# Kernel optimization log

Measured on AMD Instinct MI355X. Metric: run time of the kernel, lower is better.

## Reference

```python
import jax, jax.numpy as jnp
import numpy as np

N, E, D = 100_000, 1_250_000, 64
EPS = 1e-8

def setup_inputs() -> dict:
    key = jax.random.key(0)
    ks = jax.random.split(key, 8)
    h = jax.random.normal(ks[0], (N, D), jnp.float32)
    eig = jax.random.normal(ks[1], (E, 1), jnp.float32)          # per-edge vector field
    snorm_n = jax.random.uniform(ks[2], (N, 1), jnp.float32)     # node norm
    src = jax.random.randint(ks[3], (E,), 0, N)
    dst = jax.random.randint(ks[4], (E,), 0, N)
    # pretrans: Linear(2D -> D); posttrans: Linear((3+1)*D -> D); torch Linear weight is [out, in]
    W1 = jax.random.normal(ks[5], (D, 2 * D), jnp.float32) / np.sqrt(2.0 * D)
    b1 = jnp.zeros((D,), jnp.float32)
    W2 = jax.random.normal(ks[6], (D, 4 * D), jnp.float32) / np.sqrt(4.0 * D)
    b2 = jnp.zeros((D,), jnp.float32)
    gamma = jnp.ones((D,), jnp.float32)   # BatchNorm1d weight
    beta = jnp.zeros((D,), jnp.float32)   # BatchNorm1d bias
    return dict(h=h, eig=eig, snorm_n=snorm_n, src=src, dst=dst,
                W1=W1, b1=b1, W2=W2, b2=b2, gamma=gamma, beta=beta)

def reference(h, eig, snorm_n, src, dst, W1, b1, W2, b2, gamma, beta):
    seg = lambda x: jax.ops.segment_sum(x, dst, num_segments=N)
    # pretrans on edges: MLP(cat[h_src, h_dst])
    z2 = jnp.concatenate([h[src], h[dst]], axis=1)   # [E, 2D]
    e = z2 @ W1.T + b1                                # [E, D]
    deg = seg(jnp.ones((E, 1), e.dtype))              # [N, 1]
    # aggregator: mean
    agg_mean = seg(e) / jnp.maximum(deg, 1.0)
    # aggregator: max (empty segments -> 0)
    agg_max = jax.ops.segment_max(e, dst, num_segments=N)
    agg_max = jnp.where(deg > 0, agg_max, 0.0)
    # aggregator: directional derivative dir_dx
    absum = seg(jnp.abs(eig))                         # [N, 1] sum of |vf| per node
    w = eig / (absum[dst] + EPS)                      # [E, 1] normalized weights
    agg_dir = jnp.abs(seg(e * w) - seg(w) * h)        # [N, D]
    # posttrans on nodes
    hc = jnp.concatenate([h, agg_mean, agg_max, agg_dir], axis=1)  # [N, 4D]
    h2 = (hc @ W2.T + b2) * snorm_n
    # BatchNorm1d (training mode: batch stats, biased variance)
    mu = jnp.mean(h2, axis=0)
    var = jnp.var(h2, axis=0)
    h2 = (h2 - mu) * jax.lax.rsqrt(var + 1e-5) * gamma + beta
    h2 = jax.nn.relu(h2)
    # residual (in_dim == out_dim); dropout p=0 is identity
    return h + h2
```

## Files before the change

kernel.cpp:

```cpp
#include <hip/hip_runtime.h>
#include <math.h>

__device__ __forceinline__ float bf2f(unsigned short s) {
    return __uint_as_float(((unsigned)s) << 16);
}
__device__ __forceinline__ unsigned short f2bf(float f) {
    unsigned u = __float_as_uint(f);
    unsigned r = (u + 0x7fffu + ((u >> 16) & 1u)) >> 16;
    return (unsigned short)r;
}

typedef __attribute__((ext_vector_type(8))) short short8v;
typedef __attribute__((ext_vector_type(4))) float f32x4;


__device__ __forceinline__ void edge_rank_body(
    int bid, const int* __restrict__ dst, int* __restrict__ cursor,
    int* __restrict__ rank, int E)
{
    int t = bid * 256 + threadIdx.x;
    int base = t * 8;
    if (base >= E) return;
    if (base + 8 <= E) {
        int4 d0 = *(const int4*)(dst + base);
        int4 d1 = *(const int4*)(dst + base + 4);
        int r0 = atomicAdd(&cursor[d0.x], 1);
        int r1 = atomicAdd(&cursor[d0.y], 1);
        int r2 = atomicAdd(&cursor[d0.z], 1);
        int r3 = atomicAdd(&cursor[d0.w], 1);
        int r4 = atomicAdd(&cursor[d1.x], 1);
        int r5 = atomicAdd(&cursor[d1.y], 1);
        int r6 = atomicAdd(&cursor[d1.z], 1);
        int r7 = atomicAdd(&cursor[d1.w], 1);
        *(int4*)(rank + base)     = make_int4(r0, r1, r2, r3);
        *(int4*)(rank + base + 4) = make_int4(r4, r5, r6, r7);
    } else {
        for (int e = base; e < E; ++e)
            rank[e] = atomicAdd(&cursor[dst[e]], 1);
    }
}

__device__ __forceinline__ void hb_cast_body(
    int bid, const float* __restrict__ h, unsigned short* __restrict__ hb, long total8)
{
    long idx = (long)bid * 256 + threadIdx.x;
    if (idx >= total8) return;
    const float4 a = *(const float4*)(h + idx * 8);
    const float4 b = *(const float4*)(h + idx * 8 + 4);
    union { unsigned short s[8]; uint4 v4; } pk;
    pk.s[0] = f2bf(a.x); pk.s[1] = f2bf(a.y); pk.s[2] = f2bf(a.z); pk.s[3] = f2bf(a.w);
    pk.s[4] = f2bf(b.x); pk.s[5] = f2bf(b.y); pk.s[6] = f2bf(b.z); pk.s[7] = f2bf(b.w);
    *(uint4*)(hb + idx * 8) = pk.v4;
}

__device__ __forceinline__ void wprep_body(
    int bid, const float* __restrict__ W1, const float* __restrict__ W2,
    unsigned short* __restrict__ w1bf, unsigned short* __restrict__ w2bf)
{
    int idx = bid * 256 + threadIdx.x;
    if (idx < 128 * 64) {
        int c = idx >> 6, j = idx & 63;
        float val = (c < 64) ? W1[c * 128 + j] : W1[(c - 64) * 128 + 64 + j];
        w1bf[idx] = f2bf(val);
    } else if (idx < 128 * 64 + 64 * 256) {
        int k = idx - 128 * 64;
        w2bf[k] = f2bf(W2[k]);
    }
}

__device__ __forceinline__ void csr_scatter_body(
    int bid, const int* __restrict__ src, const int* __restrict__ dst,
    const float* __restrict__ eig, const int* __restrict__ rank,
    const int* __restrict__ offs, int2* __restrict__ csr, int E)
{
    int e = bid * 256 + threadIdx.x;
    if (e < E) {
        int dn = dst[e];
        int p = offs[dn] + rank[e];
        csr[p] = make_int2(src[e], __float_as_int(eig[e]));
    }
}

__device__ __forceinline__ void uv_mfma_body(
    int bid, const unsigned short* __restrict__ hb, const unsigned short* __restrict__ w1bf,
    const float* __restrict__ b1,
    unsigned short* __restrict__ u, unsigned short* __restrict__ v)
{
    int lane = threadIdx.x & 63;
    int wv = threadIdx.x >> 6;
    int lr = lane & 15;
    int lg = lane >> 4;

    short8v a[2][2];
#pragma unroll
    for (int rt = 0; rt < 2; ++rt)
#pragma unroll
        for (int s = 0; s < 2; ++s)
            a[rt][s] = *(const short8v*)(w1bf + (size_t)(wv * 32 + rt * 16 + lr) * 64 + s * 32 + lg * 8);

    float b1v[2][4];
#pragma unroll
    for (int rt = 0; rt < 2; ++rt) {
        if (wv >= 2) {
            float4 t4 = *(const float4*)(b1 + (wv - 2) * 32 + rt * 16 + lg * 4);
            b1v[rt][0] = t4.x; b1v[rt][1] = t4.y; b1v[rt][2] = t4.z; b1v[rt][3] = t4.w;
        } else {
            b1v[rt][0] = b1v[rt][1] = b1v[rt][2] = b1v[rt][3] = 0.f;
        }
    }

    unsigned short* outp = (wv < 2) ? u : v;
    int coff0 = (wv & 1) * 32 + lg * 4;

    int n0 = bid * 64;

    short8v bb[2][2];
    {
        const unsigned short* hp = hb + (size_t)(n0 + lr) * 64 + lg * 8;
        bb[0][0] = *(const short8v*)(hp);
        bb[0][1] = *(const short8v*)(hp + 32);
    }
#pragma unroll
    for (int t = 0; t < 4; ++t) {
        int cur = t & 1, nxt = cur ^ 1;
        if (t < 3) {
            const unsigned short* hp = hb + (size_t)(n0 + (t + 1) * 16 + lr) * 64 + lg * 8;
            bb[nxt][0] = *(const short8v*)(hp);
            bb[nxt][1] = *(const short8v*)(hp + 32);
        }
        f32x4 acc0 = {0.f, 0.f, 0.f, 0.f}, acc1 = {0.f, 0.f, 0.f, 0.f};
        acc0 = __builtin_amdgcn_mfma_f32_16x16x32_bf16(a[0][0], bb[cur][0], acc0, 0, 0, 0);
        acc1 = __builtin_amdgcn_mfma_f32_16x16x32_bf16(a[1][0], bb[cur][0], acc1, 0, 0, 0);
        acc0 = __builtin_amdgcn_mfma_f32_16x16x32_bf16(a[0][1], bb[cur][1], acc0, 0, 0, 0);
        acc1 = __builtin_amdgcn_mfma_f32_16x16x32_bf16(a[1][1], bb[cur][1], acc1, 0, 0, 0);
        int node = n0 + t * 16 + lr;
        union { unsigned short s[4]; uint2 v2; } pk;
#pragma unroll
        for (int r = 0; r < 4; ++r) pk.s[r] = f2bf(acc0[r] + b1v[0][r]);
        *(uint2*)(outp + (size_t)node * 64 + coff0) = pk.v2;
#pragma unroll
        for (int r = 0; r < 4; ++r) pk.s[r] = f2bf(acc1[r] + b1v[1][r]);
        *(uint2*)(outp + (size_t)node * 64 + coff0 + 16) = pk.v2;
    }
}

__global__ __launch_bounds__(256) void mega1_kernel(
    const int* __restrict__ dst, int* __restrict__ cursor, int* __restrict__ rank, int E,
    const float* __restrict__ h, unsigned short* __restrict__ hb, long total8,
    const float* __restrict__ W1, const float* __restrict__ W2,
    unsigned short* __restrict__ w1bf, unsigned short* __restrict__ w2bf,
    int nrank, int ncast)
{
    int b = blockIdx.x;
    if (b < nrank)              edge_rank_body(b, dst, cursor, rank, E);
    else if (b < nrank + ncast) hb_cast_body(b - nrank, h, hb, total8);
    else                        wprep_body(b - nrank - ncast, W1, W2, w1bf, w2bf);
}

__global__ __launch_bounds__(256) void mega2_kernel(
    const unsigned short* __restrict__ hb, const unsigned short* __restrict__ w1bf,
    const float* __restrict__ b1, unsigned short* __restrict__ u, unsigned short* __restrict__ v,
    const int* __restrict__ src, const int* __restrict__ dst, const float* __restrict__ eig,
    const int* __restrict__ rank, const int* __restrict__ offs, int2* __restrict__ csr,
    int E, int nuv)
{
    int b = blockIdx.x;
    if (b < nuv) uv_mfma_body(b, hb, w1bf, b1, u, v);
    else         csr_scatter_body(b - nuv, src, dst, eig, rank, offs, csr, E);
}

__global__ __launch_bounds__(256) void block_reduce_kernel(
    const int* __restrict__ deg, int* __restrict__ bsum, int N)
{
    __shared__ int sd[256];
    int t = threadIdx.x;
    int i = blockIdx.x * 256 + t;
    sd[t] = (i < N) ? deg[i] : 0;
    __syncthreads();
    for (int s = 128; s > 0; s >>= 1) {
        if (t < s) sd[t] += sd[t + s];
        __syncthreads();
    }
    if (t == 0) bsum[blockIdx.x] = sd[0];
}

__global__ __launch_bounds__(1024) void scan_bsums_kernel(
    const int* __restrict__ bsum, int* __restrict__ bscan, int nb)
{
    __shared__ int sd[1024];
    int t = threadIdx.x;
    int own = (t < nb) ? bsum[t] : 0;
    sd[t] = own;
    __syncthreads();
    for (int off = 1; off < 1024; off <<= 1) {
        int v = (t >= off) ? sd[t - off] : 0;
        __syncthreads();
        sd[t] += v;
        __syncthreads();
    }
    if (t < nb) bscan[t] = sd[t] - own;
}

__global__ __launch_bounds__(256) void block_scan_kernel(
    const int* __restrict__ deg, const int* __restrict__ bscan,
    int* __restrict__ offs, int N)
{
    __shared__ int sd[256];
    int t = threadIdx.x;
    int i = blockIdx.x * 256 + t;
    int myv = (i < N) ? deg[i] : 0;
    sd[t] = myv;
    __syncthreads();
    for (int off = 1; off < 256; off <<= 1) {
        int v = (t >= off) ? sd[t - off] : 0;
        __syncthreads();
        sd[t] += v;
        __syncthreads();
    }
    if (i < N) {
        offs[i] = sd[t] - myv + bscan[blockIdx.x];
    }
}

__global__ __launch_bounds__(256) void agg_kernel(
    const unsigned short* __restrict__ u, const unsigned short* __restrict__ v,
    const unsigned short* __restrict__ hb,
    const int* __restrict__ offs, const int* __restrict__ degi,
    const int2* __restrict__ csr,
    unsigned short* __restrict__ agg, int N)
{
    int gw = (blockIdx.x * 256 + threadIdx.x) >> 6;
    int lane = threadIdx.x & 63;
    int n = __builtin_amdgcn_readfirstlane(gw);
    if (n >= N) return;
    int dn  = __builtin_amdgcn_readfirstlane(degi[n]);
    int beg = __builtin_amdgcn_readfirstlane(offs[n]);

    float vl = bf2f(v[(size_t)n * 64 + lane]);
    float hl = bf2f(hb[(size_t)n * 64 + lane]);

    const int2* ep = csr + beg;
    float accs = 0.f, accd = 0.f, accm = -3.402823466e38f;
    float pa = 0.f, ps = 0.f;

    int j = 0;
    for (; j + 4 <= dn; j += 4) {
        int2 r0 = ep[j], r1 = ep[j + 1], r2 = ep[j + 2], r3 = ep[j + 3];
        float u0 = bf2f(u[(size_t)r0.x * 64 + lane]);
        float u1 = bf2f(u[(size_t)r1.x * 64 + lane]);
        float u2 = bf2f(u[(size_t)r2.x * 64 + lane]);
        float u3 = bf2f(u[(size_t)r3.x * 64 + lane]);
        float w0 = __int_as_float(r0.y), w1 = __int_as_float(r1.y);
        float w2_ = __int_as_float(r2.y), w3 = __int_as_float(r3.y);
        pa += (fabsf(w0) + fabsf(w1)) + (fabsf(w2_) + fabsf(w3));
        ps += (w0 + w1) + (w2_ + w3);
        accs += (u0 + u1) + (u2 + u3);
        accm = fmaxf(accm, fmaxf(fmaxf(u0, u1), fmaxf(u2, u3)));
        accd = fmaf(w0, u0, fmaf(w1, u1, fmaf(w2_, u2, fmaf(w3, u3, accd))));
    }
    for (; j < dn; ++j) {
        int2 r0 = ep[j];
        float u0 = bf2f(u[(size_t)r0.x * 64 + lane]);
        float w0 = __int_as_float(r0.y);
        pa += fabsf(w0);
        ps += w0;
        accs += u0;
        accm = fmaxf(accm, u0);
        accd = fmaf(w0, u0, accd);
    }

    float inv_ab = 1.f / (pa + 1e-8f);
    float segw = ps * inv_ab;

    float fdeg = (float)dn;
    float mean = (accs + fdeg * vl) / fmaxf(fdeg, 1.f);
    float amax = (dn > 0) ? (accm + vl) : 0.f;
    float adir = fabsf(fmaf(accd, inv_ab, segw * (vl - hl)));
    size_t base = (size_t)n * 192;
    agg[base + lane]       = f2bf(mean);
    agg[base + 64 + lane]  = f2bf(amax);
    agg[base + 128 + lane] = f2bf(adir);
}

__global__ __launch_bounds__(256) void post_mfma_kernel(
    const unsigned short* __restrict__ hb, const unsigned short* __restrict__ agg,
    const unsigned short* __restrict__ w2bf, const float* __restrict__ b2,
    const float* __restrict__ snorm, float* __restrict__ h2,
    float* __restrict__ bn_part, int N)
{
    int lane = threadIdx.x & 63;
    int w = threadIdx.x >> 6;
    int lr = lane & 15;
    int lg = lane >> 4;

    short8v a[8];
    {
        const unsigned short* ab = w2bf + ((size_t)(w * 16 + lr)) * 256 + lg * 8;
#pragma unroll
        for (int s = 0; s < 8; ++s)
            a[s] = *(const short8v*)(ab + s * 32);
    }
    float4 b2v = *(const float4*)(b2 + w * 16 + lg * 4);
    float b2a[4] = {b2v.x, b2v.y, b2v.z, b2v.w};

    int n0 = blockIdx.x * 128;
    float s1[4] = {0.f, 0.f, 0.f, 0.f}, s2[4] = {0.f, 0.f, 0.f, 0.f};

    short8v bb[2][8];
    float snv[2];

#define LOADT(BUF, T)                                                            \
    {                                                                            \
        int node_ = n0 + (T) * 16 + lr;                                          \
        const unsigned short* hbp_ = hb  + (size_t)node_ * 64  + lg * 8;         \
        const unsigned short* agp_ = agg + (size_t)node_ * 192 + lg * 8;         \
        bb[BUF][0] = *(const short8v*)(hbp_);                                    \
        bb[BUF][1] = *(const short8v*)(hbp_ + 32);                               \
        bb[BUF][2] = *(const short8v*)(agp_);                                    \
        bb[BUF][3] = *(const short8v*)(agp_ + 32);                               \
        bb[BUF][4] = *(const short8v*)(agp_ + 64);                               \
        bb[BUF][5] = *(const short8v*)(agp_ + 96);                               \
        bb[BUF][6] = *(const short8v*)(agp_ + 128);                              \
        bb[BUF][7] = *(const short8v*)(agp_ + 160);                              \
        int nc_ = (node_ < N) ? node_ : (N - 1);                                 \
        snv[BUF] = snorm[nc_];                                                   \
    }

    LOADT(0, 0)
#pragma unroll
    for (int t = 0; t < 8; ++t) {
        int cur = t & 1, nxt = cur ^ 1;
        if (t < 7) LOADT(nxt, t + 1)
        f32x4 acc0 = {0.f, 0.f, 0.f, 0.f}, acc1 = {0.f, 0.f, 0.f, 0.f};
#pragma unroll
        for (int s = 0; s < 8; s += 2) {
            acc0 = __builtin_amdgcn_mfma_f32_16x16x32_bf16(a[s],     bb[cur][s],     acc0, 0, 0, 0);
            acc1 = __builtin_amdgcn_mfma_f32_16x16x32_bf16(a[s + 1], bb[cur][s + 1], acc1, 0, 0, 0);
        }
        int node = n0 + t * 16 + lr;
        bool ok = node < N;
        float sn = snv[cur];
        float xr[4];
#pragma unroll
        for (int r = 0; r < 4; ++r) {
            float val = (acc0[r] + acc1[r] + b2a[r]) * sn;
            val = ok ? val : 0.f;
            xr[r] = val;
            s1[r] += val;
            s2[r] = fmaf(val, val, s2[r]);
        }
        *(float4*)(h2 + (size_t)node * 64 + w * 16 + lg * 4) =
            make_float4(xr[0], xr[1], xr[2], xr[3]);
    }
#undef LOADT

#pragma unroll
    for (int m = 1; m < 16; m <<= 1) {
#pragma unroll
        for (int r = 0; r < 4; ++r) {
            s1[r] += __shfl_xor(s1[r], m);
            s2[r] += __shfl_xor(s2[r], m);
        }
    }
    if (lr == 0) {
        int d = w * 16 + lg * 4;
        float* bp = bn_part + (size_t)blockIdx.x * 128;
#pragma unroll
        for (int r = 0; r < 4; ++r) {
            bp[d + r]      = s1[r];
            bp[64 + d + r] = s2[r];
        }
    }
}

__global__ __launch_bounds__(1024) void bn_reduce_kernel(
    const float* __restrict__ bn_part, const float* __restrict__ gamma,
    const float* __restrict__ beta, float* __restrict__ bn_buf, int nblk, float invN)
{
    __shared__ float sred[1024];
    int t = threadIdx.x;
    int d = t & 127;
    int sl = t >> 7;
    float s = 0.f;
    for (int b = sl; b < nblk; b += 8)
        s += bn_part[(size_t)b * 128 + d];
    sred[t] = s;
    __syncthreads();
    if (sl == 0) {
        float tot = s;
#pragma unroll
        for (int k = 1; k < 8; ++k) tot += sred[k * 128 + d];
        sred[d] = tot;
    }
    __syncthreads();
    if (t < 64) {
        float s1 = sred[t], s2 = sred[64 + t];
        float mu = s1 * invN;
        float var = s2 * invN - mu * mu;
        float rstd = rsqrtf(var + 1e-5f);
        float sc = rstd * gamma[t];
        bn_buf[t]      = sc;
        bn_buf[64 + t] = beta[t] - mu * sc;
    }
}

__global__ __launch_bounds__(256) void bn_final_kernel(
    const float* __restrict__ h, const float* __restrict__ h2,
    const float* __restrict__ bn_buf, float* __restrict__ out, int N)
{
    int idx = blockIdx.x * 256 + threadIdx.x;
    int total4 = N * 16;
    if (idx >= total4) return;
    int base = idx * 4;
    int d0 = base & 63;
    const float4 a = *(const float4*)(h2 + base);
    const float4 hh = *(const float4*)(h + base);
    float r[4] = {a.x, a.y, a.z, a.w};
    float hv[4] = {hh.x, hh.y, hh.z, hh.w};
    float o[4];
#pragma unroll
    for (int k = 0; k < 4; ++k) {
        int d = d0 + k;
        float x = fmaf(r[k], bn_buf[d], bn_buf[64 + d]);
        o[k] = hv[k] + fmaxf(x, 0.f);
    }
    float4 ov = {o[0], o[1], o[2], o[3]};
    *(float4*)(out + base) = ov;
}

extern "C" void kernel_launch(void* const* d_in, const int* in_sizes, int n_in,
                              void* d_out, int out_size, void* d_ws, size_t ws_size,
                              hipStream_t stream)
{
    const float* h     = (const float*)d_in[0];
    const float* eig   = (const float*)d_in[1];
    const float* snorm = (const float*)d_in[2];
    const int*   src   = (const int*)d_in[3];
    const int*   dst   = (const int*)d_in[4];
    const float* W1    = (const float*)d_in[5];
    const float* b1    = (const float*)d_in[6];
    const float* W2    = (const float*)d_in[7];
    const float* b2    = (const float*)d_in[8];
    const float* gamma = (const float*)d_in[9];
    const float* beta  = (const float*)d_in[10];
    float* out = (float*)d_out;

    const int N = in_sizes[2];
    const int E = in_sizes[1];
    const int Npad = (N + 255) & ~255;
    const int pblk = (N + 127) / 128;

    char* w = (char*)d_ws;
    size_t off = 0;
    auto alloc = [&](size_t bytes) -> char* {
        char* p = w + off;
        off += (bytes + 255) & ~size_t(255);
        return p;
    };
    unsigned short* u = (unsigned short*)alloc((size_t)Npad * 64 * 2);
    unsigned short* v = (unsigned short*)alloc((size_t)Npad * 64 * 2);
    float* h2 = (float*)u;
    unsigned short* agg = (unsigned short*)alloc((size_t)Npad * 192 * 2);
    unsigned short* hb  = (unsigned short*)alloc((size_t)Npad * 64 * 2);
    int2* csr = (int2*)alloc((size_t)E * 8);
    int*  rank = (int*)alloc((size_t)E * 4);
    char* zero_base = w + off;
    int*   cursor = (int*)alloc((size_t)N * 4);
    size_t zero_bytes = (size_t)((w + off) - zero_base);
    float* bn_part = (float*)alloc((size_t)pblk * 128 * 4);
    float* bn_buf  = (float*)alloc(128 * 4);
    int* offs = (int*)alloc((size_t)N * 4);
    int nb = (N + 255) / 256;
    int* bsum  = (int*)alloc((size_t)nb * 4);
    int* bscan = (int*)alloc((size_t)nb * 4);
    unsigned short* w1bf = (unsigned short*)alloc(128 * 64 * 2);
    unsigned short* w2bf = (unsigned short*)alloc(64 * 256 * 2);
    (void)ws_size; (void)n_in; (void)out_size;

    hipMemsetAsync(zero_base, 0, zero_bytes, stream);

    long total8 = (long)N * 8;
    int nrank = (E + 2047) / 2048;
    int ncast = (int)((total8 + 255) / 256);
    int nwprep = (128 * 64 + 64 * 256 + 255) / 256;
    mega1_kernel<<<nrank + ncast + nwprep, 256, 0, stream>>>(
        dst, cursor, rank, E, h, hb, total8, W1, W2, w1bf, w2bf, nrank, ncast);

    block_reduce_kernel<<<nb, 256, 0, stream>>>(cursor, bsum, N);
    scan_bsums_kernel<<<1, 1024, 0, stream>>>(bsum, bscan, nb);
    block_scan_kernel<<<nb, 256, 0, stream>>>(cursor, bscan, offs, N);

    int nuv = (N + 63) / 64;
    int nscat = (E + 255) / 256;
    mega2_kernel<<<nuv + nscat, 256, 0, stream>>>(
        hb, w1bf, b1, u, v, src, dst, eig, rank, offs, csr, E, nuv);

    int agrid = (int)(((size_t)N * 64 + 255) / 256);
    agg_kernel<<<agrid, 256, 0, stream>>>(u, v, hb, offs, cursor, csr, agg, N);

    post_mfma_kernel<<<pblk, 256, 0, stream>>>(hb, agg, w2bf, b2, snorm,
                                               h2, bn_part, N);

    bn_reduce_kernel<<<1, 1024, 0, stream>>>(bn_part, gamma, beta, bn_buf, pblk, 1.0f / (float)N);

    int fgrid = (N * 16 + 255) / 256;
    bn_final_kernel<<<fgrid, 256, 0, stream>>>(h, h2, bn_buf, out, N);
}
```

Baseline: 317.9 us.

## Fuse neighbor aggregation into posttrans MFMA kernel via shared-memory staging

Merges the per-node aggregation kernel and the posttrans MFMA kernel into one kernel. Each block aggregates 64 nodes, with each wave handling 16 nodes in sequence, and writes the bf16 mean/max/dir features into padded LDS instead of a global agg buffer. The MFMA stage then reads its B operands from LDS. This removes a kernel launch and the global write and re-read of the agg array. In exchange each wave now walks its 16 nodes serially, so fewer independent waves hide gather latency. The LDS use (about 25KB per block) may also reduce occupancy, and h2 now gets its own allocation instead of aliasing u.

```diff
diff --git a/kernel.cpp b/kernel.cpp
--- a/kernel.cpp
+++ b/kernel.cpp
@@ -222,74 +222,77 @@
     }
 }
 
-__global__ __launch_bounds__(256) void agg_kernel(
+__global__ __launch_bounds__(256) void aggpost_kernel(
     const unsigned short* __restrict__ u, const unsigned short* __restrict__ v,
     const unsigned short* __restrict__ hb,
     const int* __restrict__ offs, const int* __restrict__ degi,
     const int2* __restrict__ csr,
-    unsigned short* __restrict__ agg, int N)
-{
-    int gw = (blockIdx.x * 256 + threadIdx.x) >> 6;
-    int lane = threadIdx.x & 63;
-    int n = __builtin_amdgcn_readfirstlane(gw);
-    if (n >= N) return;
-    int dn  = __builtin_amdgcn_readfirstlane(degi[n]);
-    int beg = __builtin_amdgcn_readfirstlane(offs[n]);
-
-    float vl = bf2f(v[(size_t)n * 64 + lane]);
-    float hl = bf2f(hb[(size_t)n * 64 + lane]);
-
-    const int2* ep = csr + beg;
-    float accs = 0.f, accd = 0.f, accm = -3.402823466e38f;
-    float pa = 0.f, ps = 0.f;
-
-    int j = 0;
-    for (; j + 4 <= dn; j += 4) {
-        int2 r0 = ep[j], r1 = ep[j + 1], r2 = ep[j + 2], r3 = ep[j + 3];
-        float u0 = bf2f(u[(size_t)r0.x * 64 + lane]);
-        float u1 = bf2f(u[(size_t)r1.x * 64 + lane]);
-        float u2 = bf2f(u[(size_t)r2.x * 64 + lane]);
-        float u3 = bf2f(u[(size_t)r3.x * 64 + lane]);
-        float w0 = __int_as_float(r0.y), w1 = __int_as_float(r1.y);
-        float w2_ = __int_as_float(r2.y), w3 = __int_as_float(r3.y);
-        pa += (fabsf(w0) + fabsf(w1)) + (fabsf(w2_) + fabsf(w3));
-        ps += (w0 + w1) + (w2_ + w3);
-        accs += (u0 + u1) + (u2 + u3);
-        accm = fmaxf(accm, fmaxf(fmaxf(u0, u1), fmaxf(u2, u3)));
-        accd = fmaf(w0, u0, fmaf(w1, u1, fmaf(w2_, u2, fmaf(w3, u3, accd))));
-    }
-    for (; j < dn; ++j) {
-        int2 r0 = ep[j];
-        float u0 = bf2f(u[(size_t)r0.x * 64 + lane]);
-        float w0 = __int_as_float(r0.y);
-        pa += fabsf(w0);
-        ps += w0;
-        accs += u0;
-        accm = fmaxf(accm, u0);
-        accd = fmaf(w0, u0, accd);
-    }
-
-    float inv_ab = 1.f / (pa + 1e-8f);
-    float segw = ps * inv_ab;
-
-    float fdeg = (float)dn;
-    float mean = (accs + fdeg * vl) / fmaxf(fdeg, 1.f);
-    float amax = (dn > 0) ? (accm + vl) : 0.f;
-    float adir = fabsf(fmaf(accd, inv_ab, segw * (vl - hl)));
-    size_t base = (size_t)n * 192;
-    agg[base + lane]       = f2bf(mean);
-    agg[base + 64 + lane]  = f2bf(amax);
-    agg[base + 128 + lane] = f2bf(adir);
-}
-
-__global__ __launch_bounds__(256) void post_mfma_kernel(
-    const unsigned short* __restrict__ hb, const unsigned short* __restrict__ agg,
     const unsigned short* __restrict__ w2bf, const float* __restrict__ b2,
     const float* __restrict__ snorm, float* __restrict__ h2,
     float* __restrict__ bn_part, int N)
 {
-    int lane = threadIdx.x & 63;
-    int w = threadIdx.x >> 6;
+    __shared__ unsigned short aggL[64 * 200];
+
+    int tid = threadIdx.x;
+    int lane = tid & 63;
+    int w = tid >> 6;
+    int n0 = blockIdx.x * 64;
+
+    for (int i = 0; i < 16; ++i) {
+        int n = n0 + w * 16 + i;
+        if (n < N) {
+            int dn  = __builtin_amdgcn_readfirstlane(degi[n]);
+            int beg = __builtin_amdgcn_readfirstlane(offs[n]);
+
+            float vl = bf2f(v[(size_t)n * 64 + lane]);
+            float hl = bf2f(hb[(size_t)n * 64 + lane]);
+
+            const int2* ep = csr + beg;
+            float accs = 0.f, accd = 0.f, accm = -3.402823466e38f;
+            float pa = 0.f, ps = 0.f;
+
+            int j = 0;
+            for (; j + 4 <= dn; j += 4) {
+                int2 r0 = ep[j], r1 = ep[j + 1], r2 = ep[j + 2], r3 = ep[j + 3];
+                float u0 = bf2f(u[(size_t)r0.x * 64 + lane]);
+                float u1 = bf2f(u[(size_t)r1.x * 64 + lane]);
+                float u2 = bf2f(u[(size_t)r2.x * 64 + lane]);
+                float u3 = bf2f(u[(size_t)r3.x * 64 + lane]);
+                float w0 = __int_as_float(r0.y), w1 = __int_as_float(r1.y);
+                float w2_ = __int_as_float(r2.y), w3 = __int_as_float(r3.y);
+                pa += (fabsf(w0) + fabsf(w1)) + (fabsf(w2_) + fabsf(w3));
+                ps += (w0 + w1) + (w2_ + w3);
+                accs += (u0 + u1) + (u2 + u3);
+                accm = fmaxf(accm, fmaxf(fmaxf(u0, u1), fmaxf(u2, u3)));
+                accd = fmaf(w0, u0, fmaf(w1, u1, fmaf(w2_, u2, fmaf(w3, u3, accd))));
+            }
+            for (; j < dn; ++j) {
+                int2 r0 = ep[j];
+                float u0 = bf2f(u[(size_t)r0.x * 64 + lane]);
+                float w0 = __int_as_float(r0.y);
+                pa += fabsf(w0);
+                ps += w0;
+                accs += u0;
+                accm = fmaxf(accm, u0);
+                accd = fmaf(w0, u0, accd);
+            }
+
+            float inv_ab = 1.f / (pa + 1e-8f);
+            float segw = ps * inv_ab;
+
+            float fdeg = (float)dn;
+            float mean = (accs + fdeg * vl) / fmaxf(fdeg, 1.f);
+            float amax = (dn > 0) ? (accm + vl) : 0.f;
+            float adir = fabsf(fmaf(accd, inv_ab, segw * (vl - hl)));
+
+            int nl = w * 16 + i;
+            aggL[nl * 200 + lane]       = f2bf(mean);
+            aggL[nl * 200 + 64 + lane]  = f2bf(amax);
+            aggL[nl * 200 + 128 + lane] = f2bf(adir);
+        }
+    }
+    __syncthreads();
+
     int lr = lane & 15;
     int lg = lane >> 4;
 
@@ -303,40 +306,39 @@
     float4 b2v = *(const float4*)(b2 + w * 16 + lg * 4);
     float b2a[4] = {b2v.x, b2v.y, b2v.z, b2v.w};
 
-    int n0 = blockIdx.x * 128;
     float s1[4] = {0.f, 0.f, 0.f, 0.f}, s2[4] = {0.f, 0.f, 0.f, 0.f};
 
-    short8v bb[2][8];
+    short8v bg[2][2];
     float snv[2];
-
-#define LOADT(BUF, T)                                                            \
-    {                                                                            \
-        int node_ = n0 + (T) * 16 + lr;                                          \
-        const unsigned short* hbp_ = hb  + (size_t)node_ * 64  + lg * 8;         \
-        const unsigned short* agp_ = agg + (size_t)node_ * 192 + lg * 8;         \
-        bb[BUF][0] = *(const short8v*)(hbp_);                                    \
-        bb[BUF][1] = *(const short8v*)(hbp_ + 32);                               \
-        bb[BUF][2] = *(const short8v*)(agp_);                                    \
-        bb[BUF][3] = *(const short8v*)(agp_ + 32);                               \
-        bb[BUF][4] = *(const short8v*)(agp_ + 64);                               \
-        bb[BUF][5] = *(const short8v*)(agp_ + 96);                               \
-        bb[BUF][6] = *(const short8v*)(agp_ + 128);                              \
-        bb[BUF][7] = *(const short8v*)(agp_ + 160);                              \
-        int nc_ = (node_ < N) ? node_ : (N - 1);                                 \
-        snv[BUF] = snorm[nc_];                                                   \
-    }
-
-    LOADT(0, 0)
-#pragma unroll
-    for (int t = 0; t < 8; ++t) {
+    {
+        int node_ = n0 + lr;
+        const unsigned short* hbp_ = hb + (size_t)node_ * 64 + lg * 8;
+        bg[0][0] = *(const short8v*)(hbp_);
+        bg[0][1] = *(const short8v*)(hbp_ + 32);
+        snv[0] = snorm[(node_ < N) ? node_ : (N - 1)];
+    }
+#pragma unroll
+    for (int t = 0; t < 4; ++t) {
         int cur = t & 1, nxt = cur ^ 1;
-        if (t < 7) LOADT(nxt, t + 1)
+        if (t < 3) {
+            int node_ = n0 + (t + 1) * 16 + lr;
+            const unsigned short* hbp_ = hb + (size_t)node_ * 64 + lg * 8;
+            bg[nxt][0] = *(const short8v*)(hbp_);
+            bg[nxt][1] = *(const short8v*)(hbp_ + 32);
+            snv[nxt] = snorm[(node_ < N) ? node_ : (N - 1)];
+        }
+        int nl_ = t * 16 + lr;
+        const unsigned short* al = aggL + nl_ * 200 + lg * 8;
         f32x4 acc0 = {0.f, 0.f, 0.f, 0.f}, acc1 = {0.f, 0.f, 0.f, 0.f};
-#pragma unroll
-        for (int s = 0; s < 8; s += 2) {
-            acc0 = __builtin_amdgcn_mfma_f32_16x16x32_bf16(a[s],     bb[cur][s],     acc0, 0, 0, 0);
-            acc1 = __builtin_amdgcn_mfma_f32_16x16x32_bf16(a[s + 1], bb[cur][s + 1], acc1, 0, 0, 0);
-        }
+        acc0 = __builtin_amdgcn_mfma_f32_16x16x32_bf16(a[0], bg[cur][0], acc0, 0, 0, 0);
+        acc1 = __builtin_amdgcn_mfma_f32_16x16x32_bf16(a[1], bg[cur][1], acc1, 0, 0, 0);
+        acc0 = __builtin_amdgcn_mfma_f32_16x16x32_bf16(a[2], *(const short8v*)(al),       acc0, 0, 0, 0);
+        acc1 = __builtin_amdgcn_mfma_f32_16x16x32_bf16(a[3], *(const short8v*)(al + 32),  acc1, 0, 0, 0);
+        acc0 = __builtin_amdgcn_mfma_f32_16x16x32_bf16(a[4], *(const short8v*)(al + 64),  acc0, 0, 0, 0);
+        acc1 = __builtin_amdgcn_mfma_f32_16x16x32_bf16(a[5], *(const short8v*)(al + 96),  acc1, 0, 0, 0);
+        acc0 = __builtin_amdgcn_mfma_f32_16x16x32_bf16(a[6], *(const short8v*)(al + 128), acc0, 0, 0, 0);
+        acc1 = __builtin_amdgcn_mfma_f32_16x16x32_bf16(a[7], *(const short8v*)(al + 160), acc1, 0, 0, 0);
+
         int node = n0 + t * 16 + lr;
         bool ok = node < N;
         float sn = snv[cur];
@@ -352,7 +354,6 @@
         *(float4*)(h2 + (size_t)node * 64 + w * 16 + lg * 4) =
             make_float4(xr[0], xr[1], xr[2], xr[3]);
     }
-#undef LOADT
 
 #pragma unroll
     for (int m = 1; m < 16; m <<= 1) {
@@ -448,7 +449,7 @@
     const int N = in_sizes[2];
     const int E = in_sizes[1];
     const int Npad = (N + 255) & ~255;
-    const int pblk = (N + 127) / 128;
+    const int pblk = (N + 63) / 64;
 
     char* w = (char*)d_ws;
     size_t off = 0;
@@ -459,8 +460,7 @@
     };
     unsigned short* u = (unsigned short*)alloc((size_t)Npad * 64 * 2);
     unsigned short* v = (unsigned short*)alloc((size_t)Npad * 64 * 2);
-    float* h2 = (float*)u;
-    unsigned short* agg = (unsigned short*)alloc((size_t)Npad * 192 * 2);
+    float* h2 = (float*)alloc((size_t)Npad * 64 * 4);
     unsigned short* hb  = (unsigned short*)alloc((size_t)Npad * 64 * 2);
     int2* csr = (int2*)alloc((size_t)E * 8);
     int*  rank = (int*)alloc((size_t)E * 4);
@@ -495,11 +495,8 @@
     mega2_kernel<<<nuv + nscat, 256, 0, stream>>>(
         hb, w1bf, b1, u, v, src, dst, eig, rank, offs, csr, E, nuv);
 
-    int agrid = (int)(((size_t)N * 64 + 255) / 256);
-    agg_kernel<<<agrid, 256, 0, stream>>>(u, v, hb, offs, cursor, csr, agg, N);
-
-    post_mfma_kernel<<<pblk, 256, 0, stream>>>(hb, agg, w2bf, b2, snorm,
-                                               h2, bn_part, N);
+    aggpost_kernel<<<pblk, 256, 0, stream>>>(u, v, hb, offs, cursor, csr,
+                                             w2bf, b2, snorm, h2, bn_part, N);
 
     bn_reduce_kernel<<<1, 1024, 0, stream>>>(bn_part, gamma, beta, bn_buf, pblk, 1.0f / (float)N);
 
```

New measurement: 359.3 us. +13.0%, slower.

## Split aggregation and post-MLP into halves to overlap them in a merged kernel

Applied to the files above, without the earlier changes.

Aggregation and the post-transform MFMA GEMM are split into two node halves. The first half is aggregated alone. A merged kernel then runs the post GEMM on the first half while aggregating the second half, and a final launch runs the post GEMM on the second half. This lets the compute-heavy GEMM overlap the gather-bound aggregation. It adds one launch and gives h2 its own buffer, because it can no longer alias u while u is still being read.

```diff
diff --git a/kernel.cpp b/kernel.cpp
--- a/kernel.cpp
+++ b/kernel.cpp
@@ -144,94 +144,17 @@
     }
 }
 
-__global__ __launch_bounds__(256) void mega1_kernel(
-    const int* __restrict__ dst, int* __restrict__ cursor, int* __restrict__ rank, int E,
-    const float* __restrict__ h, unsigned short* __restrict__ hb, long total8,
-    const float* __restrict__ W1, const float* __restrict__ W2,
-    unsigned short* __restrict__ w1bf, unsigned short* __restrict__ w2bf,
-    int nrank, int ncast)
-{
-    int b = blockIdx.x;
-    if (b < nrank)              edge_rank_body(b, dst, cursor, rank, E);
-    else if (b < nrank + ncast) hb_cast_body(b - nrank, h, hb, total8);
-    else                        wprep_body(b - nrank - ncast, W1, W2, w1bf, w2bf);
-}
-
-__global__ __launch_bounds__(256) void mega2_kernel(
-    const unsigned short* __restrict__ hb, const unsigned short* __restrict__ w1bf,
-    const float* __restrict__ b1, unsigned short* __restrict__ u, unsigned short* __restrict__ v,
-    const int* __restrict__ src, const int* __restrict__ dst, const float* __restrict__ eig,
-    const int* __restrict__ rank, const int* __restrict__ offs, int2* __restrict__ csr,
-    int E, int nuv)
-{
-    int b = blockIdx.x;
-    if (b < nuv) uv_mfma_body(b, hb, w1bf, b1, u, v);
-    else         csr_scatter_body(b - nuv, src, dst, eig, rank, offs, csr, E);
-}
-
-__global__ __launch_bounds__(256) void block_reduce_kernel(
-    const int* __restrict__ deg, int* __restrict__ bsum, int N)
-{
-    __shared__ int sd[256];
-    int t = threadIdx.x;
-    int i = blockIdx.x * 256 + t;
-    sd[t] = (i < N) ? deg[i] : 0;
-    __syncthreads();
-    for (int s = 128; s > 0; s >>= 1) {
-        if (t < s) sd[t] += sd[t + s];
-        __syncthreads();
-    }
-    if (t == 0) bsum[blockIdx.x] = sd[0];
-}
-
-__global__ __launch_bounds__(1024) void scan_bsums_kernel(
-    const int* __restrict__ bsum, int* __restrict__ bscan, int nb)
-{
-    __shared__ int sd[1024];
-    int t = threadIdx.x;
-    int own = (t < nb) ? bsum[t] : 0;
-    sd[t] = own;
-    __syncthreads();
-    for (int off = 1; off < 1024; off <<= 1) {
-        int v = (t >= off) ? sd[t - off] : 0;
-        __syncthreads();
-        sd[t] += v;
-        __syncthreads();
-    }
-    if (t < nb) bscan[t] = sd[t] - own;
-}
-
-__global__ __launch_bounds__(256) void block_scan_kernel(
-    const int* __restrict__ deg, const int* __restrict__ bscan,
-    int* __restrict__ offs, int N)
-{
-    __shared__ int sd[256];
-    int t = threadIdx.x;
-    int i = blockIdx.x * 256 + t;
-    int myv = (i < N) ? deg[i] : 0;
-    sd[t] = myv;
-    __syncthreads();
-    for (int off = 1; off < 256; off <<= 1) {
-        int v = (t >= off) ? sd[t - off] : 0;
-        __syncthreads();
-        sd[t] += v;
-        __syncthreads();
-    }
-    if (i < N) {
-        offs[i] = sd[t] - myv + bscan[blockIdx.x];
-    }
-}
-
-__global__ __launch_bounds__(256) void agg_kernel(
+__device__ __forceinline__ void agg_body(
+    int bid, int nbase,
     const unsigned short* __restrict__ u, const unsigned short* __restrict__ v,
     const unsigned short* __restrict__ hb,
     const int* __restrict__ offs, const int* __restrict__ degi,
     const int2* __restrict__ csr,
     unsigned short* __restrict__ agg, int N)
 {
-    int gw = (blockIdx.x * 256 + threadIdx.x) >> 6;
+    int gw = (bid * 256 + (int)threadIdx.x) >> 6;
     int lane = threadIdx.x & 63;
-    int n = __builtin_amdgcn_readfirstlane(gw);
+    int n = __builtin_amdgcn_readfirstlane(nbase + gw);
     if (n >= N) return;
     int dn  = __builtin_amdgcn_readfirstlane(degi[n]);
     int beg = __builtin_amdgcn_readfirstlane(offs[n]);
@@ -282,7 +205,8 @@
     agg[base + 128 + lane] = f2bf(adir);
 }
 
-__global__ __launch_bounds__(256) void post_mfma_kernel(
+__device__ __forceinline__ void post_body(
+    int pb,
     const unsigned short* __restrict__ hb, const unsigned short* __restrict__ agg,
     const unsigned short* __restrict__ w2bf, const float* __restrict__ b2,
     const float* __restrict__ snorm, float* __restrict__ h2,
@@ -303,7 +227,7 @@
     float4 b2v = *(const float4*)(b2 + w * 16 + lg * 4);
     float b2a[4] = {b2v.x, b2v.y, b2v.z, b2v.w};
 
-    int n0 = blockIdx.x * 128;
+    int n0 = pb * 128;
     float s1[4] = {0.f, 0.f, 0.f, 0.f}, s2[4] = {0.f, 0.f, 0.f, 0.f};
 
     short8v bb[2][8];
@@ -364,12 +288,125 @@
     }
     if (lr == 0) {
         int d = w * 16 + lg * 4;
-        float* bp = bn_part + (size_t)blockIdx.x * 128;
+        float* bp = bn_part + (size_t)pb * 128;
 #pragma unroll
         for (int r = 0; r < 4; ++r) {
             bp[d + r]      = s1[r];
             bp[64 + d + r] = s2[r];
         }
+    }
+}
+
+__global__ __launch_bounds__(256) void mega1_kernel(
+    const int* __restrict__ dst, int* __restrict__ cursor, int* __restrict__ rank, int E,
+    const float* __restrict__ h, unsigned short* __restrict__ hb, long total8,
+    const float* __restrict__ W1, const float* __restrict__ W2,
+    unsigned short* __restrict__ w1bf, unsigned short* __restrict__ w2bf,
+    int nrank, int ncast)
+{
+    int b = blockIdx.x;
+    if (b < nrank)              edge_rank_body(b, dst, cursor, rank, E);
+    else if (b < nrank + ncast) hb_cast_body(b - nrank, h, hb, total8);
+    else                        wprep_body(b - nrank - ncast, W1, W2, w1bf, w2bf);
+}
+
+__global__ __launch_bounds__(256) void mega2_kernel(
+    const unsigned short* __restrict__ hb, const unsigned short* __restrict__ w1bf,
+    const float* __restrict__ b1, unsigned short* __restrict__ u, unsigned short* __restrict__ v,
+    const int* __restrict__ src, const int* __restrict__ dst, const float* __restrict__ eig,
+    const int* __restrict__ rank, const int* __restrict__ offs, int2* __restrict__ csr,
+    int E, int nuv)
+{
+    int b = blockIdx.x;
+    if (b < nuv) uv_mfma_body(b, hb, w1bf, b1, u, v);
+    else         csr_scatter_body(b - nuv, src, dst, eig, rank, offs, csr, E);
+}
+
+__global__ __launch_bounds__(256) void mega3_kernel(
+    const unsigned short* __restrict__ hb, const unsigned short* __restrict__ aggbuf,
+    const unsigned short* __restrict__ w2bf, const float* __restrict__ b2,
+    const float* __restrict__ snorm, float* __restrict__ h2,
+    float* __restrict__ bn_part,
+    const unsigned short* __restrict__ u, const unsigned short* __restrict__ v,
+    const int* __restrict__ offs, const int* __restrict__ degi,
+    const int2* __restrict__ csr,
+    int N, int npost, int agg_nbase)
+{
+    int b = blockIdx.x;
+    if (b < npost) post_body(b, hb, aggbuf, w2bf, b2, snorm, h2, bn_part, N);
+    else           agg_body(b - npost, agg_nbase, u, v, hb, offs, degi, csr,
+                            (unsigned short*)aggbuf, N);
+}
+
+__global__ __launch_bounds__(256) void agg_kernel(
+    const unsigned short* __restrict__ u, const unsigned short* __restrict__ v,
+    const unsigned short* __restrict__ hb,
+    const int* __restrict__ offs, const int* __restrict__ degi,
+    const int2* __restrict__ csr,
+    unsigned short* __restrict__ agg, int N)
+{
+    agg_body(blockIdx.x, 0, u, v, hb, offs, degi, csr, agg, N);
+}
+
+__global__ __launch_bounds__(256) void post_mfma_kernel(
+    const unsigned short* __restrict__ hb, const unsigned short* __restrict__ agg,
+    const unsigned short* __restrict__ w2bf, const float* __restrict__ b2,
+    const float* __restrict__ snorm, float* __restrict__ h2,
+    float* __restrict__ bn_part, int N, int boff)
+{
+    post_body(blockIdx.x + boff, hb, agg, w2bf, b2, snorm, h2, bn_part, N);
+}
+
+__global__ __launch_bounds__(256) void block_reduce_kernel(
+    const int* __restrict__ deg, int* __restrict__ bsum, int N)
+{
+    __shared__ int sd[256];
+    int t = threadIdx.x;
+    int i = blockIdx.x * 256 + t;
+    sd[t] = (i < N) ? deg[i] : 0;
+    __syncthreads();
+    for (int s = 128; s > 0; s >>= 1) {
+        if (t < s) sd[t] += sd[t + s];
+        __syncthreads();
+    }
+    if (t == 0) bsum[blockIdx.x] = sd[0];
+}
+
+__global__ __launch_bounds__(1024) void scan_bsums_kernel(
+    const int* __restrict__ bsum, int* __restrict__ bscan, int nb)
+{
+    __shared__ int sd[1024];
+    int t = threadIdx.x;
+    int own = (t < nb) ? bsum[t] : 0;
+    sd[t] = own;
+    __syncthreads();
+    for (int off = 1; off < 1024; off <<= 1) {
+        int v = (t >= off) ? sd[t - off] : 0;
+        __syncthreads();
+        sd[t] += v;
+        __syncthreads();
+    }
+    if (t < nb) bscan[t] = sd[t] - own;
+}
+
+__global__ __launch_bounds__(256) void block_scan_kernel(
+    const int* __restrict__ deg, const int* __restrict__ bscan,
+    int* __restrict__ offs, int N)
+{
+    __shared__ int sd[256];
+    int t = threadIdx.x;
+    int i = blockIdx.x * 256 + t;
+    int myv = (i < N) ? deg[i] : 0;
+    sd[t] = myv;
+    __syncthreads();
+    for (int off = 1; off < 256; off <<= 1) {
+        int v = (t >= off) ? sd[t - off] : 0;
+        __syncthreads();
+        sd[t] += v;
+        __syncthreads();
+    }
+    if (i < N) {
+        offs[i] = sd[t] - myv + bscan[blockIdx.x];
     }
 }
 
@@ -459,7 +496,7 @@
     };
     unsigned short* u = (unsigned short*)alloc((size_t)Npad * 64 * 2);
     unsigned short* v = (unsigned short*)alloc((size_t)Npad * 64 * 2);
-    float* h2 = (float*)u;
+    float* h2 = (float*)alloc((size_t)Npad * 64 * 4);
     unsigned short* agg = (unsigned short*)alloc((size_t)Npad * 192 * 2);
     unsigned short* hb  = (unsigned short*)alloc((size_t)Npad * 64 * 2);
     int2* csr = (int2*)alloc((size_t)E * 8);
@@ -495,11 +532,26 @@
     mega2_kernel<<<nuv + nscat, 256, 0, stream>>>(
         hb, w1bf, b1, u, v, src, dst, eig, rank, offs, csr, E, nuv);
 
-    int agrid = (int)(((size_t)N * 64 + 255) / 256);
-    agg_kernel<<<agrid, 256, 0, stream>>>(u, v, hb, offs, cursor, csr, agg, N);
-
-    post_mfma_kernel<<<pblk, 256, 0, stream>>>(hb, agg, w2bf, b2, snorm,
-                                               h2, bn_part, N);
+    if (pblk >= 2) {
+        int pblkA = pblk / 2;
+        int nhalf = pblkA * 128;
+        int aggA = (nhalf + 3) / 4;
+        int naggB_nodes = N - nhalf;
+        int aggB = (naggB_nodes + 3) / 4;
+        int pblkB = pblk - pblkA;
+
+        agg_kernel<<<aggA, 256, 0, stream>>>(u, v, hb, offs, cursor, csr, agg, N);
+        mega3_kernel<<<pblkA + aggB, 256, 0, stream>>>(
+            hb, agg, w2bf, b2, snorm, h2, bn_part,
+            u, v, offs, cursor, csr, N, pblkA, nhalf);
+        post_mfma_kernel<<<pblkB, 256, 0, stream>>>(hb, agg, w2bf, b2, snorm,
+                                                    h2, bn_part, N, pblkA);
+    } else {
+        int agrid = (N + 3) / 4;
+        agg_kernel<<<agrid, 256, 0, stream>>>(u, v, hb, offs, cursor, csr, agg, N);
+        post_mfma_kernel<<<pblk, 256, 0, stream>>>(hb, agg, w2bf, b2, snorm,
+                                                   h2, bn_part, N, 0);
+    }
 
     bn_reduce_kernel<<<1, 1024, 0, stream>>>(bn_part, gamma, beta, bn_buf, pblk, 1.0f / (float)N);
 
```

Result: slower. 353.7 us (+11.3%).
